# Kernel tuning notes

Hardware: AMD Instinct MI355X
Metric: run time of the kernel (lower is better)

The kernel has to match this reference:

```python
import jax, jax.numpy as jnp
import numpy as np

N_NODES = 100000
N_EDGES = 1600000
N_GRAPHS = 64
D_IN = 128
D_HID = 128
D_OUT = 4
LEAKY_SLOPE = 0.01  # nn.LeakyReLU default


def setup_inputs() -> dict:
    key = jax.random.key(0)
    k1, k2, k3, k4, k5 = jax.random.split(key, 5)
    x = jax.random.normal(k1, (N_NODES, D_IN), dtype=jnp.float32)
    edge_index = jax.random.randint(k2, (2, N_EDGES), 0, N_NODES, dtype=jnp.int32)
    batch = jnp.sort(jax.random.randint(k3, (N_NODES,), 0, N_GRAPHS, dtype=jnp.int32))
    s1 = 1.0 / np.sqrt(D_IN)
    W1 = jax.random.uniform(k4, (D_IN, D_HID), jnp.float32, -s1, s1)
    b1 = jnp.zeros((D_HID,), jnp.float32)
    W2 = jax.random.uniform(k5, (D_HID, D_OUT), jnp.float32, -s1, s1)
    b2 = jnp.zeros((D_OUT,), jnp.float32)
    return {"x": x, "edge_index": edge_index, "batch": batch,
            "W1": W1, "b1": b1, "W2": W2, "b2": b2}


def _gcn_conv(x, src, dst, norm, W, b, n_nodes):
    # h = X W; messages = norm * h[src]; aggregate at dst; add bias
    h = x @ W
    msg = h[src] * norm[:, None]
    agg = jax.ops.segment_sum(msg, dst, num_segments=n_nodes)
    return agg + b


def reference(x, edge_index, batch, W1, b1, W2, b2):
    n = x.shape[0]
    # add self-loops (PyG GCNConv default)
    loops = jnp.arange(n, dtype=edge_index.dtype)
    src = jnp.concatenate([edge_index[0], loops])
    dst = jnp.concatenate([edge_index[1], loops])
    # symmetric normalization: deg over target index, weight 1
    deg = jax.ops.segment_sum(jnp.ones_like(src, dtype=x.dtype), dst, num_segments=n)
    deg_is = jnp.where(deg > 0, jax.lax.rsqrt(deg), 0.0)
    norm = deg_is[src] * deg_is[dst]

    h = _gcn_conv(x, src, dst, norm, W1, b1, n)
    h = jnp.where(h >= 0, h, LEAKY_SLOPE * h)  # LeakyReLU
    # dropout is identity at inference
    h = _gcn_conv(h, src, dst, norm, W2, b2, n)

    # global mean pool over graphs
    sums = jax.ops.segment_sum(h, batch, num_segments=N_GRAPHS)
    cnts = jax.ops.segment_sum(jnp.ones((n,), h.dtype), batch, num_segments=N_GRAPHS)
    pooled = sums / jnp.maximum(cnts, 1.0)[:, None]
    return jax.nn.softmax(pooled, axis=1)
```

## Files before the change

### kernel.cpp

```cpp
#include <hip/hip_runtime.h>

#define D 128
#define NG 64
#define NPB 256
#define MAXBK 512
#define CAPB 8192
#define PCHUNK 4096
#define PLCAP 5376
#define ENTCAP 21
#define NPASS 4
#define LDA 136

typedef unsigned int uint;
typedef unsigned short ushort_t;
typedef unsigned char uchar_t;
typedef float v2f __attribute__((ext_vector_type(2)));
typedef short s8v __attribute__((ext_vector_type(8)));
typedef float f4v __attribute__((ext_vector_type(4)));

__device__ __forceinline__ uint bfr(float x) {
    uint u = __float_as_uint(x);
    return (u + 0x7FFFu + ((u >> 16) & 1u)) >> 16;
}

__global__ __launch_bounds__(512) void k_init(int* __restrict__ gcur, float* __restrict__ psum,
                                              float* __restrict__ pcnt, int NBK) {
    int t = threadIdx.x;
    if (t < NBK) gcur[t] = t * CAPB;
    if (t < NG * 4) psum[t] = 0.f;
    if (t < NG) pcnt[t] = 0.f;
}

__global__ __launch_bounds__(256) void k_prep(const float* __restrict__ W,
                                              short* __restrict__ W1T) {
    int idx = blockIdx.x * 256 + threadIdx.x;
    int nn = idx >> 7, kk = idx & 127;
    W1T[idx] = (short)bfr(W[kk * D + nn]);
}

__global__ __launch_bounds__(256) void k_part(const int* __restrict__ edge,
                                              int* __restrict__ gcur, int* __restrict__ p1,
                                              int E, int NBK) {
    __shared__ int hist[MAXBK], scn[MAXBK], curb[MAXBK], fixb[MAXBK];
    __shared__ int ps[256];
    __shared__ int sortb[PCHUNK];
    __shared__ ushort_t sbkt[PCHUNK];
    int tid = threadIdx.x;
    for (int i = tid; i < MAXBK; i += 256) { hist[i] = 0; curb[i] = 0; }
    __syncthreads();
    int lo = blockIdx.x * PCHUNK;
    int hi = min(lo + PCHUNK, E);
    int cnt = hi - lo;
    for (int e = lo + tid; e < hi; e += 256) atomicAdd(&hist[edge[E + e] >> 8], 1);
    __syncthreads();
    int a = hist[2 * tid], b = hist[2 * tid + 1];
    ps[tid] = a + b;
    __syncthreads();
    for (int o = 1; o < 256; o <<= 1) {
        int x = (tid >= o) ? ps[tid - o] : 0;
        __syncthreads();
        ps[tid] += x;
        __syncthreads();
    }
    int pe = ps[tid] - (a + b);
    scn[2 * tid] = pe;
    scn[2 * tid + 1] = pe + a;
    __syncthreads();
    for (int bk = tid; bk < NBK; bk += 256)
        if (hist[bk]) fixb[bk] = atomicAdd(&gcur[bk], hist[bk]) - scn[bk];
    __syncthreads();
    for (int e = lo + tid; e < hi; e += 256) {
        int s = edge[e];
        int d2 = edge[E + e];
        int bk = d2 >> 8;
        int r = scn[bk] + atomicAdd(&curb[bk], 1);
        sortb[r] = ((d2 & 255) << 17) | s;
        sbkt[r] = (ushort_t)bk;
    }
    __syncthreads();
    for (int p = tid; p < cnt; p += 256) {
        int bk = sbkt[p];
        p1[fixb[bk] + p] = sortb[p];
    }
}

__global__ __launch_bounds__(256) void k_place(const int* __restrict__ p1,
                                               const int* __restrict__ gcur,
                                               int* __restrict__ ed, int2* __restrict__ offdeg,
                                               float* __restrict__ dinv, int n) {
    __shared__ int cnts[256], scn[256], cur[256];
    __shared__ int outb[PLCAP];
    int tid = threadIdx.x;
    int b = blockIdx.x;
    int base = b * CAPB;
    int cnt = gcur[b] - base;
    int end = base + cnt;
    int node0 = b << 8;
    cnts[tid] = 0;
    cur[tid] = 0;
    __syncthreads();
    int ent[ENTCAP];
    int ne = 0;
    for (int p = base + tid; p < end; p += 256) {
        int v = p1[p];
        if (ne < ENTCAP) ent[ne] = v;
        ne++;
        atomicAdd(&cnts[v >> 17], 1);
    }
    __syncthreads();
    int v0 = cnts[tid];
    scn[tid] = v0;
    __syncthreads();
    for (int o = 1; o < 256; o <<= 1) {
        int x = (tid >= o) ? scn[tid - o] : 0;
        __syncthreads();
        scn[tid] += x;
        __syncthreads();
    }
    int excl = scn[tid] - v0;
    int node = node0 + tid;
    if (node < n) {
        offdeg[node] = make_int2(base + excl, v0);
        dinv[node] = rsqrtf((float)(v0 + 1));
    }
    scn[tid] = excl;
    __syncthreads();
    int m = (ne < ENTCAP) ? ne : ENTCAP;
    for (int k = 0; k < m; ++k) {
        int v = ent[k];
        int l = v >> 17;
        int r = scn[l] + atomicAdd(&cur[l], 1);
        if (r < PLCAP) outb[r] = v & 0x1FFFF;
        else ed[base + r] = v & 0x1FFFF;
    }
    for (int p = base + tid + ENTCAP * 256; p < end; p += 256) {
        int v = p1[p];
        int l = v >> 17;
        int r = scn[l] + atomicAdd(&cur[l], 1);
        if (r < PLCAP) outb[r] = v & 0x1FFFF;
        else ed[base + r] = v & 0x1FFFF;
    }
    __syncthreads();
    int lim = (cnt < PLCAP) ? cnt : PLCAP;
    for (int p = tid; p < lim; p += 256) ed[base + p] = outb[p];
}

__global__ __launch_bounds__(256) void k_gemm_mfma(const float* __restrict__ X,
                                                   const short* __restrict__ W1T,
                                                   const float* __restrict__ dinv,
                                                   uchar_t* __restrict__ H8b, int M) {
    __shared__ short sA[128 * LDA];
    __shared__ short sB[128 * LDA];
    __shared__ float sDinv[128];
    const int tid = threadIdx.x;
    const int blockM = blockIdx.x * 128;

    if (tid < 128) {
        int gm = blockM + tid;
        sDinv[tid] = (gm < M) ? dinv[gm] : 0.f;
    }
    {
        int c = tid & 31, g = tid >> 5;
#pragma unroll
        for (int i = 0; i < 16; ++i) {
            int r = g + i * 8;
            int gm = blockM + r;
            float4 v = make_float4(0, 0, 0, 0);
            if (gm < M) v = *(const float4*)&X[(size_t)gm * D + c * 4];
            uint lo = bfr(v.x) | (bfr(v.y) << 16);
            uint hi = bfr(v.z) | (bfr(v.w) << 16);
            *(uint2*)&sA[r * LDA + c * 4] = make_uint2(lo, hi);
        }
    }
    {
        int nn = tid >> 1, seg = tid & 1;
        const short* src = W1T + nn * 128 + seg * 64;
        short* dst = &sB[nn * LDA + seg * 64];
#pragma unroll
        for (int i = 0; i < 8; ++i)
            *(int4*)&dst[i * 8] = *(const int4*)&src[i * 8];
    }
    __syncthreads();

    const int wv = tid >> 6;
    const int lane = tid & 63;
    const int m0w = (wv >> 1) * 64, n0w = (wv & 1) * 64;
    const int mrow = lane & 15;
    const int quad = lane >> 4;

    f4v acc[4][4];
#pragma unroll
    for (int mi = 0; mi < 4; ++mi)
#pragma unroll
        for (int ni = 0; ni < 4; ++ni) acc[mi][ni] = (f4v)(0.f);

#pragma unroll
    for (int ks = 0; ks < 4; ++ks) {
        s8v af[4], bf[4];
#pragma unroll
        for (int mi = 0; mi < 4; ++mi)
            af[mi] = *(const s8v*)&sA[(m0w + mi * 16 + mrow) * LDA + ks * 32 + quad * 8];
#pragma unroll
        for (int ni = 0; ni < 4; ++ni)
            bf[ni] = *(const s8v*)&sB[(n0w + ni * 16 + mrow) * LDA + ks * 32 + quad * 8];
#pragma unroll
        for (int mi = 0; mi < 4; ++mi)
#pragma unroll
            for (int ni = 0; ni < 4; ++ni)
                acc[mi][ni] = __builtin_amdgcn_mfma_f32_16x16x32_bf16(af[mi], bf[ni], acc[mi][ni], 0, 0, 0);
    }

#pragma unroll
    for (int mi = 0; mi < 4; ++mi) {
#pragma unroll
        for (int r = 0; r < 4; ++r) {
            int lrow = m0w + mi * 16 + quad * 4 + r;
            int gm = blockM + lrow;
            if (gm >= M) continue;
            float di = sDinv[lrow];
#pragma unroll
            for (int ni = 0; ni < 4; ++ni) {
                int col = n0w + ni * 16 + mrow;
                float v = acc[mi][ni][r] * di;
                uint p = __builtin_amdgcn_cvt_pk_fp8_f32(v, v, 0u, false);
                H8b[((size_t)(col >> 5) * M + gm) * 32 + (col & 31)] = (uchar_t)(p & 0xFF);
            }
        }
    }
}

__global__ __launch_bounds__(256) void k_gather_pass(const uint* __restrict__ Hsu,
                                                     const int2* __restrict__ offdeg,
                                                     const int* __restrict__ ed,
                                                     const float* __restrict__ dinv,
                                                     const float* __restrict__ b1,
                                                     const float* __restrict__ W2,
                                                     float4* __restrict__ zpart,
                                                     float4* __restrict__ zs,
                                                     int n, int p) {
    __shared__ float sW[128];
    __shared__ float sb[32];
    int tid = threadIdx.x;
    if (tid < 128) sW[tid] = W2[p * 128 + tid];
    if (tid < 32) sb[tid] = b1[p * 32 + tid];
    __syncthreads();
    int node = blockIdx.x * 32 + (tid >> 3);
    if (node >= n) return;
    int lane = tid & 7;
    const uint* T = Hsu + (size_t)p * n * 8;
    float di = dinv[node];
    uint h0 = T[(node << 3) + lane];
    v2f lo = __builtin_amdgcn_cvt_pk_f32_fp8(h0, false);
    v2f hi = __builtin_amdgcn_cvt_pk_f32_fp8(h0, true);
    float acc0 = lo.x, acc1 = lo.y, acc2 = hi.x, acc3 = hi.y;
    int2 od = offdeg[node];
    int j0 = od.x, j1 = od.x + od.y;
    int j = j0;
    for (; j + 8 <= j1; j += 8) {
        uint r[8];
#pragma unroll
        for (int k = 0; k < 8; ++k) r[k] = T[(ed[j + k] << 3) + lane];
#pragma unroll
        for (int k = 0; k < 8; ++k) {
            v2f l2 = __builtin_amdgcn_cvt_pk_f32_fp8(r[k], false);
            v2f h2 = __builtin_amdgcn_cvt_pk_f32_fp8(r[k], true);
            acc0 += l2.x; acc1 += l2.y; acc2 += h2.x; acc3 += h2.y;
        }
    }
    for (; j < j1; ++j) {
        uint rr = T[(ed[j] << 3) + lane];
        v2f l2 = __builtin_amdgcn_cvt_pk_f32_fp8(rr, false);
        v2f h2 = __builtin_amdgcn_cvt_pk_f32_fp8(rr, true);
        acc0 += l2.x; acc1 += l2.y; acc2 += h2.x; acc3 += h2.y;
    }
    int f = lane * 4;
    float v0 = di * acc0 + sb[f + 0];
    float v1 = di * acc1 + sb[f + 1];
    float v2 = di * acc2 + sb[f + 2];
    float v3 = di * acc3 + sb[f + 3];
    v0 = v0 >= 0.f ? v0 : 0.01f * v0;
    v1 = v1 >= 0.f ? v1 : 0.01f * v1;
    v2 = v2 >= 0.f ? v2 : 0.01f * v2;
    v3 = v3 >= 0.f ? v3 : 0.01f * v3;
    float a0 = v0 * sW[f * 4 + 0] + v1 * sW[(f + 1) * 4 + 0] + v2 * sW[(f + 2) * 4 + 0] + v3 * sW[(f + 3) * 4 + 0];
    float a1 = v0 * sW[f * 4 + 1] + v1 * sW[(f + 1) * 4 + 1] + v2 * sW[(f + 2) * 4 + 1] + v3 * sW[(f + 3) * 4 + 1];
    float a2 = v0 * sW[f * 4 + 2] + v1 * sW[(f + 1) * 4 + 2] + v2 * sW[(f + 2) * 4 + 2] + v3 * sW[(f + 3) * 4 + 2];
    float a3 = v0 * sW[f * 4 + 3] + v1 * sW[(f + 1) * 4 + 3] + v2 * sW[(f + 2) * 4 + 3] + v3 * sW[(f + 3) * 4 + 3];
#pragma unroll
    for (int o = 4; o >= 1; o >>= 1) {
        a0 += __shfl_xor(a0, o);
        a1 += __shfl_xor(a1, o);
        a2 += __shfl_xor(a2, o);
        a3 += __shfl_xor(a3, o);
    }
    if (lane == 0) {
        if (p < 3) {
            zpart[(size_t)p * n + node] = make_float4(a0, a1, a2, a3);
        } else {
            float4 q0 = zpart[node];
            float4 q1 = zpart[(size_t)n + node];
            float4 q2 = zpart[(size_t)2 * n + node];
            zs[node] = make_float4(di * (a0 + q0.x + q1.x + q2.x), di * (a1 + q0.y + q1.y + q2.y),
                                   di * (a2 + q0.z + q1.z + q2.z), di * (a3 + q0.w + q1.w + q2.w));
        }
    }
}

__global__ __launch_bounds__(256) void k_pool2(const int* __restrict__ p1,
                                               const int* __restrict__ gcur,
                                               const float4* __restrict__ zs,
                                               const float* __restrict__ dinv,
                                               const int* __restrict__ batch,
                                               float* __restrict__ psum, float* __restrict__ pcnt,
                                               int n) {
    __shared__ float ls[NG * 4];
    __shared__ float lc[NG];
    __shared__ float dinvd[NPB];
    __shared__ int gl[NPB];
    int tid = threadIdx.x;
    int b = blockIdx.x >> 1;
    int half = blockIdx.x & 1;
    int node0 = b << 8;
    int node = node0 + tid;
    ls[tid] = 0.f;
    if (tid < NG) lc[tid] = 0.f;
    bool valid = node < n;
    float di = valid ? dinv[node] : 0.f;
    int g = valid ? batch[node] : -1;
    dinvd[tid] = di;
    gl[tid] = g;
    __syncthreads();
    float a0 = 0.f, a1 = 0.f, a2 = 0.f, a3 = 0.f;
    int cg = -1;
    if (half == 0 && valid) {
        float4 zv = zs[node];
        cg = g;
        a0 = di * zv.x; a1 = di * zv.y; a2 = di * zv.z; a3 = di * zv.w;
        atomicAdd(&lc[g], 1.f);
    }
    int base = b * CAPB;
    int cnt = gcur[b] - base;
    int mid = cnt >> 1;
    int s0 = base + (half ? mid : 0);
    int s1 = base + (half ? cnt : mid);
    for (int p = s0 + tid; p < s1; p += 1024) {
        int vv[4];
        float4 zb[4];
        int nb = 0;
#pragma unroll
        for (int k = 0; k < 4; ++k) {
            int q = p + k * 256;
            if (q < s1) vv[nb++] = p1[q];
        }
#pragma unroll
        for (int k = 0; k < 4; ++k)
            if (k < nb) zb[k] = zs[vv[k] & 0x1FFFF];
#pragma unroll
        for (int k = 0; k < 4; ++k) {
            if (k >= nb) continue;
            int dl = vv[k] >> 17;
            float w = dinvd[dl];
            int eg = gl[dl];
            if (eg != cg) {
                if (cg >= 0) {
                    atomicAdd(&ls[cg * 4 + 0], a0);
                    atomicAdd(&ls[cg * 4 + 1], a1);
                    atomicAdd(&ls[cg * 4 + 2], a2);
                    atomicAdd(&ls[cg * 4 + 3], a3);
                }
                cg = eg;
                a0 = a1 = a2 = a3 = 0.f;
            }
            a0 += w * zb[k].x; a1 += w * zb[k].y; a2 += w * zb[k].z; a3 += w * zb[k].w;
        }
    }
    if (cg >= 0) {
        atomicAdd(&ls[cg * 4 + 0], a0);
        atomicAdd(&ls[cg * 4 + 1], a1);
        atomicAdd(&ls[cg * 4 + 2], a2);
        atomicAdd(&ls[cg * 4 + 3], a3);
    }
    __syncthreads();
    atomicAdd(&psum[tid], ls[tid]);
    if (tid < NG) atomicAdd(&pcnt[tid], lc[tid]);
}

__global__ void k_final(const float* __restrict__ psum, const float* __restrict__ pcnt,
                        const float* __restrict__ b2, float* __restrict__ out) {
    int g = threadIdx.x;
    float c = fmaxf(pcnt[g], 1.f);
    float inv = 1.f / c;
    float l0 = psum[g * 4 + 0] * inv + b2[0];
    float l1 = psum[g * 4 + 1] * inv + b2[1];
    float l2 = psum[g * 4 + 2] * inv + b2[2];
    float l3 = psum[g * 4 + 3] * inv + b2[3];
    float m = fmaxf(fmaxf(l0, l1), fmaxf(l2, l3));
    float e0 = expf(l0 - m), e1 = expf(l1 - m), e2 = expf(l2 - m), e3 = expf(l3 - m);
    float s = 1.f / (e0 + e1 + e2 + e3);
    *(float4*)&out[g * 4] = make_float4(e0 * s, e1 * s, e2 * s, e3 * s);
}

extern "C" void kernel_launch(void* const* d_in, const int* in_sizes, int n_in,
                              void* d_out, int out_size, void* d_ws, size_t ws_size,
                              hipStream_t stream) {
    const float* X = (const float*)d_in[0];
    const int* edge = (const int*)d_in[1];
    const int* batch = (const int*)d_in[2];
    const float* W1 = (const float*)d_in[3];
    const float* b1 = (const float*)d_in[4];
    const float* W2 = (const float*)d_in[5];
    const float* b2 = (const float*)d_in[6];
    float* out = (float*)d_out;
    const int n = in_sizes[2];
    const int E = in_sizes[1] / 2;
    const int NBK = (n + NPB - 1) / NPB;

    uint* Hs = (uint*)d_ws;
    int* p1 = (int*)(Hs + (size_t)n * 32);
    int* ed = p1 + (size_t)NBK * CAPB;
    float4* zpart = (float4*)(ed + (size_t)NBK * CAPB);
    float4* zs = zpart + (size_t)NPASS * n;
    float* dinv = (float*)(zs + n);
    int2* offdeg = (int2*)(dinv + n);
    short* W1T = (short*)(offdeg + n);
    int* gcur = (int*)(W1T + 16384);
    float* psum = (float*)(gcur + MAXBK);
    float* pcnt = psum + NG * 4;

    const int NP = (E + PCHUNK - 1) / PCHUNK;

    k_init<<<1, 512, 0, stream>>>(gcur, psum, pcnt, NBK);
    k_prep<<<64, 256, 0, stream>>>(W1, W1T);
    k_part<<<NP, 256, 0, stream>>>(edge, gcur, p1, E, NBK);
    k_place<<<NBK, 256, 0, stream>>>(p1, gcur, ed, offdeg, dinv, n);

    k_gemm_mfma<<<(n + 127) / 128, 256, 0, stream>>>(X, W1T, dinv, (uchar_t*)Hs, n);

    for (int p = 0; p < NPASS; ++p)
        k_gather_pass<<<(n + 31) / 32, 256, 0, stream>>>(Hs, offdeg, ed, dinv, b1, W2,
                                                         zpart, zs, n, p);

    k_pool2<<<NBK * 2, 256, 0, stream>>>(p1, gcur, zs, dinv, batch, psum, pcnt, n);
    k_final<<<1, 64, 0, stream>>>(psum, pcnt, b2, out);
}
```

Baseline: 264.1 us.

## Merge four gather passes into one interleaved launch plus a reduction kernel

```diff
diff --git a/kernel.cpp b/kernel.cpp
--- a/kernel.cpp
+++ b/kernel.cpp
@@ -23,19 +23,13 @@
     return (u + 0x7FFFu + ((u >> 16) & 1u)) >> 16;
 }
 
-__global__ __launch_bounds__(512) void k_init(int* __restrict__ gcur, float* __restrict__ psum,
-                                              float* __restrict__ pcnt, int NBK) {
-    int t = threadIdx.x;
-    if (t < NBK) gcur[t] = t * CAPB;
-    if (t < NG * 4) psum[t] = 0.f;
-    if (t < NG) pcnt[t] = 0.f;
-}
-
-__global__ __launch_bounds__(256) void k_prep(const float* __restrict__ W,
-                                              short* __restrict__ W1T) {
+__global__ __launch_bounds__(256) void k_init(const float* __restrict__ W,
+                                              short* __restrict__ W1T,
+                                              int* __restrict__ gcur, int NBK) {
     int idx = blockIdx.x * 256 + threadIdx.x;
     int nn = idx >> 7, kk = idx & 127;
     W1T[idx] = (short)bfr(W[kk * D + nn]);
+    if (idx < NBK) gcur[idx] = idx * CAPB;
 }
 
 __global__ __launch_bounds__(256) void k_part(const int* __restrict__ edge,
@@ -229,22 +223,22 @@
     }
 }
 
-__global__ __launch_bounds__(256) void k_gather_pass(const uint* __restrict__ Hsu,
-                                                     const int2* __restrict__ offdeg,
-                                                     const int* __restrict__ ed,
-                                                     const float* __restrict__ dinv,
-                                                     const float* __restrict__ b1,
-                                                     const float* __restrict__ W2,
-                                                     float4* __restrict__ zpart,
-                                                     float4* __restrict__ zs,
-                                                     int n, int p) {
+__global__ __launch_bounds__(256) void k_gather(const uint* __restrict__ Hsu,
+                                                const int2* __restrict__ offdeg,
+                                                const int* __restrict__ ed,
+                                                const float* __restrict__ dinv,
+                                                const float* __restrict__ b1,
+                                                const float* __restrict__ W2,
+                                                float4* __restrict__ zpart,
+                                                int n) {
     __shared__ float sW[128];
     __shared__ float sb[32];
     int tid = threadIdx.x;
+    int p = blockIdx.x & 3;
     if (tid < 128) sW[tid] = W2[p * 128 + tid];
     if (tid < 32) sb[tid] = b1[p * 32 + tid];
     __syncthreads();
-    int node = blockIdx.x * 32 + (tid >> 3);
+    int node = (blockIdx.x >> 2) * 32 + (tid >> 3);
     if (node >= n) return;
     int lane = tid & 7;
     const uint* T = Hsu + (size_t)p * n * 8;
@@ -293,17 +287,28 @@
         a2 += __shfl_xor(a2, o);
         a3 += __shfl_xor(a3, o);
     }
-    if (lane == 0) {
-        if (p < 3) {
-            zpart[(size_t)p * n + node] = make_float4(a0, a1, a2, a3);
-        } else {
-            float4 q0 = zpart[node];
-            float4 q1 = zpart[(size_t)n + node];
-            float4 q2 = zpart[(size_t)2 * n + node];
-            zs[node] = make_float4(di * (a0 + q0.x + q1.x + q2.x), di * (a1 + q0.y + q1.y + q2.y),
-                                   di * (a2 + q0.z + q1.z + q2.z), di * (a3 + q0.w + q1.w + q2.w));
-        }
-    }
+    if (lane == 0) zpart[(size_t)p * n + node] = make_float4(a0, a1, a2, a3);
+}
+
+__global__ __launch_bounds__(256) void k_zred(const float4* __restrict__ zpart,
+                                              const float* __restrict__ dinv,
+                                              float4* __restrict__ zs,
+                                              float* __restrict__ psum,
+                                              float* __restrict__ pcnt, int n) {
+    int tid = threadIdx.x;
+    if (blockIdx.x == 0) {
+        if (tid < NG * 4) psum[tid] = 0.f;
+        if (tid < NG) pcnt[tid] = 0.f;
+    }
+    int i = blockIdx.x * 256 + tid;
+    if (i >= n) return;
+    float4 a = zpart[i];
+    float4 b = zpart[(size_t)n + i];
+    float4 c = zpart[(size_t)2 * n + i];
+    float4 d = zpart[(size_t)3 * n + i];
+    float di = dinv[i];
+    zs[i] = make_float4(di * (a.x + b.x + c.x + d.x), di * (a.y + b.y + c.y + d.y),
+                        di * (a.z + b.z + c.z + d.z), di * (a.w + b.w + c.w + d.w));
 }
 
 __global__ __launch_bounds__(256) void k_pool2(const int* __restrict__ p1,
@@ -428,17 +433,16 @@
     float* pcnt = psum + NG * 4;
 
     const int NP = (E + PCHUNK - 1) / PCHUNK;
-
-    k_init<<<1, 512, 0, stream>>>(gcur, psum, pcnt, NBK);
-    k_prep<<<64, 256, 0, stream>>>(W1, W1T);
+    const int NGB = (n + 31) / 32;
+
+    k_init<<<64, 256, 0, stream>>>(W1, W1T, gcur, NBK);
     k_part<<<NP, 256, 0, stream>>>(edge, gcur, p1, E, NBK);
     k_place<<<NBK, 256, 0, stream>>>(p1, gcur, ed, offdeg, dinv, n);
 
     k_gemm_mfma<<<(n + 127) / 128, 256, 0, stream>>>(X, W1T, dinv, (uchar_t*)Hs, n);
 
-    for (int p = 0; p < NPASS; ++p)
-        k_gather_pass<<<(n + 31) / 32, 256, 0, stream>>>(Hs, offdeg, ed, dinv, b1, W2,
-                                                         zpart, zs, n, p);
+    k_gather<<<NGB * NPASS, 256, 0, stream>>>(Hs, offdeg, ed, dinv, b1, W2, zpart, n);
+    k_zred<<<(n + 255) / 256, 256, 0, stream>>>(zpart, dinv, zs, psum, pcnt, n);
 
     k_pool2<<<NBK * 2, 256, 0, stream>>>(p1, gcur, zs, dinv, batch, psum, pcnt, n);
     k_final<<<1, 64, 0, stream>>>(psum, pcnt, b2, out);
```

Result: faster. 242.0 us (-8.4%).
